# Kernel tuning notes

Hardware: AMD Instinct MI355X
Metric: run time of the kernel (lower is better)

Reference implementation:

```python
import jax, jax.numpy as jnp
import numpy as np

N = 50000   # nodes
E = 800000  # edges (avg degree 16)
F_IN = 128
H = 128
L = 4
LN_EPS = 1e-5


def setup_inputs() -> dict:
    key = jax.random.key(0)
    ks = jax.random.split(key, 4)
    x = jax.random.normal(ks[0], (N, F_IN), dtype=jnp.float32)
    edge_index = jax.random.randint(ks[1], (2, E), 0, N)
    conv_w = jax.random.normal(ks[2], (L, F_IN, H), dtype=jnp.float32) * 0.05
    conv_b = jnp.zeros((L, H), dtype=jnp.float32)
    ln_g = jnp.ones((L, H), dtype=jnp.float32)
    ln_b = jnp.zeros((L, H), dtype=jnp.float32)
    head_w = jax.random.normal(ks[3], (H, 1), dtype=jnp.float32) * 0.05
    head_b = jnp.zeros((1,), dtype=jnp.float32)
    return {"x": x, "edge_index": edge_index, "conv_w": conv_w, "conv_b": conv_b,
            "ln_g": ln_g, "ln_b": ln_b, "head_w": head_w, "head_b": head_b}


def _layer_norm(h, g, b):
    mu = jnp.mean(h, axis=-1, keepdims=True)
    var = jnp.mean(jnp.square(h - mu), axis=-1, keepdims=True)
    return (h - mu) * jax.lax.rsqrt(var + LN_EPS) * g + b


def _gcn_conv(h, W, b, src, dst, inv_sqrt_deg, inv_deg):
    # PyG GCNConv: self-loops + symmetric normalization D^-1/2 (A+I) D^-1/2, then bias.
    hw = h @ W  # (N, H)
    norm = inv_sqrt_deg[src] * inv_sqrt_deg[dst]  # (E,)
    msg = hw[src] * norm[:, None]  # gather + edgewise scale
    agg = jax.ops.segment_sum(msg, dst, num_segments=N)  # scatter-add
    agg = agg + hw * inv_deg[:, None]  # self-loop term (norm = 1/deg)
    return agg + b


def reference(x, edge_index, conv_w, conv_b, ln_g, ln_b, head_w, head_b):
    src, dst = edge_index[0], edge_index[1]
    # degree on target nodes, including self-loop
    deg = jax.ops.segment_sum(jnp.ones((E,), x.dtype), dst, num_segments=N) + 1.0
    inv_sqrt_deg = jax.lax.rsqrt(deg)
    inv_deg = 1.0 / deg
    h = x
    for i in range(L):
        h = _gcn_conv(h, conv_w[i], conv_b[i], src, dst, inv_sqrt_deg, inv_deg)
        h = _layer_norm(h, ln_g[i], ln_b[i])
        if i != L - 1:
            h = jax.nn.gelu(h, approximate=False)
            # dropout is identity in eval mode
    scores = (h @ head_w + head_b).squeeze(-1)  # (N,)
    return scores, h
```

## Files before the change

kernel.cpp:

```cpp
#include <hip/hip_runtime.h>
#include <math.h>

#define N_NODES 50000
#define N_EDGES 800000
#define HDIM 128
#define NLAYERS 4
#define LN_EPS 1e-5f
#define EHALF (N_EDGES / 2)
#define SEG 64
#define FILLB ((EHALF + 255) / 256)
#define GEMMB ((N_NODES + 63) / 64)
#define LFB ((N_NODES + 31) / 32)

typedef __attribute__((ext_vector_type(8))) short short8;
typedef __attribute__((ext_vector_type(4))) float floatx4;

__device__ __forceinline__ ushort f2bf(float x) {
    unsigned b = __float_as_uint(x);
    unsigned r = b + 0x7fffu + ((b >> 16) & 1u);
    return (ushort)(r >> 16);
}
__device__ __forceinline__ float2 bf2f2(unsigned u) {
    return make_float2(__uint_as_float(u << 16), __uint_as_float(u & 0xffff0000u));
}

__global__ __launch_bounds__(256) void prep_kernel(const float* __restrict__ W,
                                                   ushort* __restrict__ bfrag,
                                                   int* __restrict__ cnt) {
    int idx = blockIdx.x * 256 + threadIdx.x;
    if (idx < N_NODES) cnt[idx] = 0;
    if (idx < NLAYERS * 4 * 8 * 64) {
        int lane = idx & 63;
        int t = (idx >> 6) & 7;
        int s = (idx >> 9) & 3;
        int l = idx >> 11;
        int n = t * 16 + (lane & 15);
        int kb = s * 32 + (lane >> 4) * 8;
        const float* Wl = W + (size_t)l * HDIM * HDIM;
        union { uint4 q; ushort u[8]; } o;
#pragma unroll
        for (int j = 0; j < 8; ++j) o.u[j] = f2bf(Wl[(size_t)(kb + j) * HDIM + n]);
        *(uint4*)&bfrag[(size_t)idx * 8] = o.q;
    }
}

__device__ __forceinline__ void fill_body(int bid, int tid, const int* __restrict__ src,
                                          const int* __restrict__ dst, int* __restrict__ cnt,
                                          ushort* __restrict__ csr16) {
    int t = bid * 256 + tid;
    if (t >= EHALF) return;
    int s0 = src[t],         d0 = dst[t];
    int s1 = src[t + EHALF], d1 = dst[t + EHALF];
    int p0 = atomicAdd(&cnt[d0], 1);
    int p1 = atomicAdd(&cnt[d1], 1);
    if (p0 < SEG) csr16[d0 * SEG + p0] = (ushort)s0;
    if (p1 < SEG) csr16[d1 * SEG + p1] = (ushort)s1;
}

template <bool A_FP32>
__device__ __forceinline__ void gemm_body(int bid, int tid, const void* __restrict__ Av,
                                          const ushort* __restrict__ bfrag,
                                          ushort* __restrict__ out) {
    int wave = tid >> 6, lane = tid & 63;
    int quad = lane >> 4, mrow = lane & 15;
    int rowBase = bid * 64 + wave * 16;
    int arow = rowBase + mrow;
    bool aok = arow < N_NODES;

    floatx4 acc[8];
#pragma unroll
    for (int t = 0; t < 8; ++t) acc[t] = (floatx4)0.f;

#pragma unroll
    for (int s = 0; s < 4; ++s) {
        union { short8 v; ushort u[8]; } af;
        if (A_FP32) {
            const float* A = (const float*)Av;
            if (aok) {
                const float* p = &A[(size_t)arow * HDIM + s * 32 + quad * 8];
#pragma unroll
                for (int j = 0; j < 8; ++j) af.u[j] = f2bf(p[j]);
            } else {
#pragma unroll
                for (int j = 0; j < 8; ++j) af.u[j] = 0;
            }
        } else {
            const ushort* A = (const ushort*)Av;
            if (aok) {
                af.v = *(const short8*)&A[(size_t)arow * HDIM + s * 32 + quad * 8];
            } else {
#pragma unroll
                for (int j = 0; j < 8; ++j) af.u[j] = 0;
            }
        }
#pragma unroll
        for (int t = 0; t < 8; ++t) {
            short8 bf = *(const short8*)&bfrag[(size_t)(((s * 8 + t) * 64) + lane) * 8];
            acc[t] = __builtin_amdgcn_mfma_f32_16x16x32_bf16(af.v, bf, acc[t], 0, 0, 0);
        }
    }
#pragma unroll
    for (int t = 0; t < 8; ++t) {
#pragma unroll
        for (int r = 0; r < 4; ++r) {
            int row = rowBase + quad * 4 + r;
            if (row < N_NODES) out[(size_t)row * HDIM + t * 16 + mrow] = f2bf(acc[t][r]);
        }
    }
}

__global__ __launch_bounds__(256) void fused0_kernel(
    const int* __restrict__ src, const int* __restrict__ dst, int* __restrict__ cnt,
    ushort* __restrict__ csr16, const float* __restrict__ x,
    const ushort* __restrict__ bfrag0, ushort* __restrict__ hw) {
    if (blockIdx.x < FILLB)
        fill_body(blockIdx.x, threadIdx.x, src, dst, cnt, csr16);
    else
        gemm_body<true>(blockIdx.x - FILLB, threadIdx.x, x, bfrag0, hw);
}

__global__ __launch_bounds__(256) void agg_ln_kernel(
    const uint2* __restrict__ hw2, const int* __restrict__ degcnt,
    const ushort* __restrict__ csr16, const float* __restrict__ conv_b,
    const float* __restrict__ ln_g, const float* __restrict__ ln_b,
    uint2* __restrict__ hout_bf, float* __restrict__ hout_f32,
    const float* __restrict__ head_w, const float* __restrict__ head_b,
    float* __restrict__ scores, int final_layer) {
    int wave = threadIdx.x >> 6;
    int lane = threadIdx.x & 63;
    int g = lane >> 5;
    int li = lane & 31;
    int n = blockIdx.x * 4 + wave;
    if (n >= N_NODES) return;
    int c = li * 4;

    int rawc = degcnt[n];
    float dsum = (float)rawc + 1.0f;
    float isd_n = rsqrtf(dsum);
    float ind_n = isd_n * isd_n;
    int rs = n * SEG;
    int deg = min(rawc, SEG);

    float e0 = 0.f, e1 = 0.f, e2 = 0.f, e3 = 0.f;
    int sj = 0;
    float wj = 0.f;
    if (lane < deg) sj = (int)csr16[rs + lane];
    {
        float w = rsqrtf((float)degcnt[sj] + 1.0f);
        wj = (lane < deg) ? w : 0.f;
    }
    for (int j = 0; j < deg; j += 8) {
#pragma unroll
        for (int t = 0; t < 4; ++t) {
            int idx = j + 2 * t + g;
            int s = __shfl(sj, idx);
            float w = __shfl(wj, idx);
            uint2 u = hw2[(size_t)s * 32 + li];
            float2 q0 = bf2f2(u.x), q1 = bf2f2(u.y);
            e0 = fmaf(q0.x, w, e0); e1 = fmaf(q0.y, w, e1);
            e2 = fmaf(q1.x, w, e2); e3 = fmaf(q1.y, w, e3);
        }
    }
    e0 += __shfl_xor(e0, 32); e1 += __shfl_xor(e1, 32);
    e2 += __shfl_xor(e2, 32); e3 += __shfl_xor(e3, 32);

    uint2 hv = hw2[(size_t)n * 32 + li];
    float2 h0 = bf2f2(hv.x), h1 = bf2f2(hv.y);
    float4 cb = *(const float4*)&conv_b[c];
    float a0 = fmaf(e0, isd_n, fmaf(h0.x, ind_n, cb.x));
    float a1 = fmaf(e1, isd_n, fmaf(h0.y, ind_n, cb.y));
    float a2 = fmaf(e2, isd_n, fmaf(h1.x, ind_n, cb.z));
    float a3 = fmaf(e3, isd_n, fmaf(h1.y, ind_n, cb.w));

    float sum = a0 + a1 + a2 + a3;
#pragma unroll
    for (int o = 1; o < 32; o <<= 1) sum += __shfl_xor(sum, o);
    float mu = sum * (1.0f / HDIM);
    float d0 = a0 - mu, d1 = a1 - mu, d2 = a2 - mu, d3 = a3 - mu;
    float vs = d0 * d0 + d1 * d1 + d2 * d2 + d3 * d3;
#pragma unroll
    for (int o = 1; o < 32; o <<= 1) vs += __shfl_xor(vs, o);
    float rstd = rsqrtf(vs * (1.0f / HDIM) + LN_EPS);
    float4 gv = *(const float4*)&ln_g[c];
    float4 bv = *(const float4*)&ln_b[c];
    float y0 = fmaf(d0 * rstd, gv.x, bv.x);
    float y1 = fmaf(d1 * rstd, gv.y, bv.y);
    float y2 = fmaf(d2 * rstd, gv.z, bv.z);
    float y3 = fmaf(d3 * rstd, gv.w, bv.w);

    if (!final_layer) {
#define GELU(v) ((v) = 0.5f * (v) * (1.0f + erff((v) * 0.70710678118654752f)))
        GELU(y0); GELU(y1); GELU(y2); GELU(y3);
#undef GELU
        if (g == 0) {
            uint2 ov;
            ov.x = (unsigned)f2bf(y0) | ((unsigned)f2bf(y1) << 16);
            ov.y = (unsigned)f2bf(y2) | ((unsigned)f2bf(y3) << 16);
            hout_bf[(size_t)n * 32 + li] = ov;
        }
    } else {
        if (g == 0)
            *(float4*)&hout_f32[(size_t)n * HDIM + c] = make_float4(y0, y1, y2, y3);
        float4 hwv = *(const float4*)&head_w[c];
        float p = y0 * hwv.x + y1 * hwv.y + y2 * hwv.z + y3 * hwv.w;
#pragma unroll
        for (int o = 1; o < 32; o <<= 1) p += __shfl_xor(p, o);
        if (lane == 0) scores[n] = p + head_b[0];
    }
}

__global__ __launch_bounds__(512) void layer_fused_kernel(
    const uint2* __restrict__ h2, const int* __restrict__ degcnt,
    const ushort* __restrict__ csr16, const ushort* __restrict__ bfrag,
    const float* __restrict__ conv_b, const float* __restrict__ ln_g,
    const float* __restrict__ ln_b, uint2* __restrict__ hout_bf,
    float* __restrict__ hout_f32, const float* __restrict__ head_w,
    const float* __restrict__ head_b, float* __restrict__ scores,
    int final_layer) {
    __shared__ float aggsf[32][132];
    int wave = threadIdx.x >> 6, lane = threadIdx.x & 63;
    int g = lane >> 5, li = lane & 31;

    int nodeBase = blockIdx.x * 32 + wave * 4;
    int cnt_c = 0, sj_c = 0;
    float wj_c = 0.f;
    if (nodeBase < N_NODES) {
        cnt_c = degcnt[nodeBase];
        int degp = min(cnt_c, SEG);
        int sraw = (int)csr16[nodeBase * SEG + lane];
        sj_c = (lane < degp) ? sraw : 0;
        float w = rsqrtf((float)degcnt[sj_c] + 1.0f);
        wj_c = (lane < degp) ? w : 0.f;
    }
    for (int it = 0; it < 4; ++it) {
        int n = nodeBase + it;
        int deg = min(cnt_c, SEG), sj = sj_c;
        float dsum = (float)cnt_c + 1.0f;
        float wj = wj_c;
        int cnt_nx = 0, sraw_nx = 0;
        if (it < 3 && (n + 1) < N_NODES) {
            cnt_nx = degcnt[n + 1];
            sraw_nx = (int)csr16[(n + 1) * SEG + lane];
        }
        float a0 = 0.f, a1 = 0.f, a2 = 0.f, a3 = 0.f;
        if (n < N_NODES) {
            float isd_n = rsqrtf(dsum);
            float ind_n = isd_n * isd_n;
            uint2 hv = h2[(size_t)n * 32 + li];
            float e0 = 0.f, e1 = 0.f, e2 = 0.f, e3 = 0.f;
            uint2 u[4];
#pragma unroll
            for (int t = 0; t < 4; ++t) {
                int s = __shfl(sj, 2 * t + g);
                u[t] = h2[(size_t)s * 32 + li];
            }
            for (int j = 0; j < deg; j += 8) {
                uint2 un[4];
                int jn = j + 8;
                bool more = jn < deg;
                if (more) {
#pragma unroll
                    for (int t = 0; t < 4; ++t) {
                        int s = __shfl(sj, jn + 2 * t + g);
                        un[t] = h2[(size_t)s * 32 + li];
                    }
                }
#pragma unroll
                for (int t = 0; t < 4; ++t) {
                    float w = __shfl(wj, j + 2 * t + g);
                    float2 q0 = bf2f2(u[t].x), q1 = bf2f2(u[t].y);
                    e0 = fmaf(q0.x, w, e0); e1 = fmaf(q0.y, w, e1);
                    e2 = fmaf(q1.x, w, e2); e3 = fmaf(q1.y, w, e3);
                }
                if (more) { u[0] = un[0]; u[1] = un[1]; u[2] = un[2]; u[3] = un[3]; }
            }
            e0 += __shfl_xor(e0, 32); e1 += __shfl_xor(e1, 32);
            e2 += __shfl_xor(e2, 32); e3 += __shfl_xor(e3, 32);
            float2 h0 = bf2f2(hv.x), h1v = bf2f2(hv.y);
            a0 = fmaf(e0, isd_n, h0.x * ind_n);
            a1 = fmaf(e1, isd_n, h0.y * ind_n);
            a2 = fmaf(e2, isd_n, h1v.x * ind_n);
            a3 = fmaf(e3, isd_n, h1v.y * ind_n);
        }
        if (g == 0)
            *(float4*)&aggsf[wave * 4 + it][li * 4] = make_float4(a0, a1, a2, a3);
        int degp = min(cnt_nx, SEG);
        cnt_c = cnt_nx;
        sj_c = (lane < degp) ? sraw_nx : 0;
        float w = rsqrtf((float)degcnt[sj_c] + 1.0f);
        wj_c = (lane < degp) ? w : 0.f;
    }
    __syncthreads();

    int quad = lane >> 4, mrow = lane & 15;
    int rtile = (wave >> 2) * 16;
    int cq2 = (wave & 3) * 2;
    floatx4 acc[2];
    acc[0] = (floatx4)0.f;
    acc[1] = (floatx4)0.f;
#pragma unroll
    for (int s = 0; s < 4; ++s) {
        const float* rowp = &aggsf[rtile + mrow][s * 32 + quad * 8];
        float4 pa = *(const float4*)rowp;
        float4 pb = *(const float4*)(rowp + 4);
        float p[8] = {pa.x, pa.y, pa.z, pa.w, pb.x, pb.y, pb.z, pb.w};
        union { short8 v; ushort u[8]; } hi, lo;
#pragma unroll
        for (int j = 0; j < 8; ++j) {
            ushort h = f2bf(p[j]);
            hi.u[j] = h;
            float hf = __uint_as_float((unsigned)h << 16);
            lo.u[j] = f2bf(p[j] - hf);
        }
#pragma unroll
        for (int t4 = 0; t4 < 2; ++t4) {
            int t = cq2 + t4;
            short8 bf = *(const short8*)&bfrag[(size_t)(((s * 8 + t) * 64) + lane) * 8];
            acc[t4] = __builtin_amdgcn_mfma_f32_16x16x32_bf16(lo.v, bf, acc[t4], 0, 0, 0);
            acc[t4] = __builtin_amdgcn_mfma_f32_16x16x32_bf16(hi.v, bf, acc[t4], 0, 0, 0);
        }
    }
    __syncthreads();

    {
        float cb[2];
#pragma unroll
        for (int t4 = 0; t4 < 2; ++t4) cb[t4] = conv_b[(cq2 + t4) * 16 + mrow];
#pragma unroll
        for (int t4 = 0; t4 < 2; ++t4)
#pragma unroll
            for (int r = 0; r < 4; ++r)
                aggsf[rtile + quad * 4 + r][(cq2 + t4) * 16 + mrow] = acc[t4][r] + cb[t4];
    }
    __syncthreads();

    int c = li * 4;
    float4 gv = *(const float4*)&ln_g[c];
    float4 bv = *(const float4*)&ln_b[c];
    float4 hwv = *(const float4*)&head_w[c];
    for (int it = 0; it < 4; ++it) {
        int row = wave * 4 + it;
        int n = blockIdx.x * 32 + row;
        if (n >= N_NODES) continue;
        float4 v = *(const float4*)&aggsf[row][c];
        float a0 = v.x, a1 = v.y, a2 = v.z, a3 = v.w;

        float sum = a0 + a1 + a2 + a3;
#pragma unroll
        for (int o = 1; o < 32; o <<= 1) sum += __shfl_xor(sum, o);
        float mu = sum * (1.0f / HDIM);
        float d0 = a0 - mu, d1 = a1 - mu, d2 = a2 - mu, d3 = a3 - mu;
        float vs = d0 * d0 + d1 * d1 + d2 * d2 + d3 * d3;
#pragma unroll
        for (int o = 1; o < 32; o <<= 1) vs += __shfl_xor(vs, o);
        float rstd = rsqrtf(vs * (1.0f / HDIM) + LN_EPS);
        float y0 = fmaf(d0 * rstd, gv.x, bv.x);
        float y1 = fmaf(d1 * rstd, gv.y, bv.y);
        float y2 = fmaf(d2 * rstd, gv.z, bv.z);
        float y3 = fmaf(d3 * rstd, gv.w, bv.w);

        if (!final_layer) {
#define GELU(v) ((v) = 0.5f * (v) * (1.0f + erff((v) * 0.70710678118654752f)))
            GELU(y0); GELU(y1); GELU(y2); GELU(y3);
#undef GELU
            if (g == 0) {
                uint2 ov;
                ov.x = (unsigned)f2bf(y0) | ((unsigned)f2bf(y1) << 16);
                ov.y = (unsigned)f2bf(y2) | ((unsigned)f2bf(y3) << 16);
                hout_bf[(size_t)n * 32 + li] = ov;
            }
        } else {
            if (g == 0)
                *(float4*)&hout_f32[(size_t)n * HDIM + c] = make_float4(y0, y1, y2, y3);
            float p = y0 * hwv.x + y1 * hwv.y + y2 * hwv.z + y3 * hwv.w;
#pragma unroll
            for (int o = 1; o < 32; o <<= 1) p += __shfl_xor(p, o);
            if (lane == 0) scores[n] = p + head_b[0];
        }
    }
}


extern "C" void kernel_launch(void* const* d_in, const int* in_sizes, int n_in,
                              void* d_out, int out_size, void* d_ws, size_t ws_size,
                              hipStream_t stream) {
    const float* x      = (const float*)d_in[0];
    const int*   eidx   = (const int*)d_in[1];
    const float* conv_w = (const float*)d_in[2];
    const float* conv_b = (const float*)d_in[3];
    const float* ln_g   = (const float*)d_in[4];
    const float* ln_b   = (const float*)d_in[5];
    const float* head_w = (const float*)d_in[6];
    const float* head_b = (const float*)d_in[7];
    float* out = (float*)d_out;

    const int* src = eidx;
    const int* dst = eidx + N_EDGES;

    char* ws = (char*)d_ws;
    size_t o = 0;
    auto alloc = [&](size_t elems) {
        void* p = ws + o * 4;
        o += (elems + 15) & ~(size_t)15;
        return p;
    };
    int*      cnt      = (int*)alloc(N_NODES);
    ushort*   csr16    = (ushort*)alloc((size_t)N_NODES * SEG / 2);
    ushort*   bfrag    = (ushort*)alloc(NLAYERS * 4 * 8 * 64 * 8 / 2);
    unsigned* hw       = (unsigned*)alloc((size_t)N_NODES * 64);
    unsigned* hbuf     = (unsigned*)alloc((size_t)N_NODES * 64);

    prep_kernel<<<(N_NODES + 255) / 256, 256, 0, stream>>>(conv_w, bfrag, cnt);
    fused0_kernel<<<FILLB + GEMMB, 256, 0, stream>>>(src, dst, cnt, csr16, x, bfrag,
                                                     (ushort*)hw);

    agg_ln_kernel<<<(N_NODES + 3) / 4, 256, 0, stream>>>(
        (const uint2*)hw, cnt, csr16,
        conv_b, ln_g, ln_b,
        (uint2*)hbuf, out + N_NODES, head_w, head_b, out, 0);

    const unsigned* hin = hbuf;
    unsigned* hnext = hw;
    for (int l = 1; l < NLAYERS; ++l) {
        const ushort* bl = bfrag + (size_t)l * 4 * 8 * 64 * 8;
        int fin = (l == NLAYERS - 1) ? 1 : 0;
        layer_fused_kernel<<<LFB, 512, 0, stream>>>(
            (const uint2*)hin, cnt, csr16, bl,
            conv_b + (size_t)l * HDIM, ln_g + (size_t)l * HDIM, ln_b + (size_t)l * HDIM,
            (uint2*)hnext, out + N_NODES, head_w, head_b, out, fin);
        const unsigned* tmp = hin;
        hin = hnext;
        hnext = (unsigned*)tmp;
    }
}
```

Baseline: 340.2 us.

## Fuse all GCN layers into one persistent cooperative kernel with grid sync

Replaces the four per-layer kernel launches with a single cooperative persistent kernel. Blocks pull 32-node tiles through an atomic work cursor and separate layers with grid.sync(). The intent is to remove launch gaps and tail effects between layers and to balance irregular degree work dynamically. In exchange the grid is capped by occupancy, grid-wide barriers are added, and if the cooperative launch fails the code falls back to the old per-layer launches.

New measurement: 622.3 us. 82.9% more time.

```diff
diff --git a/kernel.cpp b/kernel.cpp
--- a/kernel.cpp
+++ b/kernel.cpp
@@ -1,5 +1,8 @@
 #include <hip/hip_runtime.h>
+#include <hip/hip_cooperative_groups.h>
 #include <math.h>
+
+namespace cg = cooperative_groups;
 
 #define N_NODES 50000
 #define N_EDGES 800000
@@ -26,9 +29,11 @@
 
 __global__ __launch_bounds__(256) void prep_kernel(const float* __restrict__ W,
                                                    ushort* __restrict__ bfrag,
-                                                   int* __restrict__ cnt) {
+                                                   int* __restrict__ cnt,
+                                                   int* __restrict__ cursor) {
     int idx = blockIdx.x * 256 + threadIdx.x;
     if (idx < N_NODES) cnt[idx] = 0;
+    if (idx < NLAYERS) cursor[idx] = 0;
     if (idx < NLAYERS * 4 * 8 * 64) {
         int lane = idx & 63;
         int t = (idx >> 6) & 7;
@@ -117,6 +122,231 @@
         fill_body(blockIdx.x, threadIdx.x, src, dst, cnt, csr16);
     else
         gemm_body<true>(blockIdx.x - FILLB, threadIdx.x, x, bfrag0, hw);
+}
+
+__global__ __launch_bounds__(512) void layers_kernel(
+    unsigned* __restrict__ hw, unsigned* __restrict__ hbuf,
+    const int* __restrict__ degcnt, const ushort* __restrict__ csr16,
+    const ushort* __restrict__ bfrag, const float* __restrict__ conv_b,
+    const float* __restrict__ ln_g, const float* __restrict__ ln_b,
+    const float* __restrict__ head_w, const float* __restrict__ head_b,
+    float* __restrict__ out, int* __restrict__ cursor) {
+    cg::grid_group grid = cg::this_grid();
+    __shared__ float aggsf[32][132];
+    __shared__ int tile_s;
+    int wave = threadIdx.x >> 6, lane = threadIdx.x & 63;
+    int g = lane >> 5, li = lane & 31;
+    int quad = lane >> 4, mrow = lane & 15;
+    float* scores = out;
+    float* hout_f32 = out + N_NODES;
+
+    for (int l = 0; l < NLAYERS; ++l) {
+        const uint2* h2 = (const uint2*)((l & 1) ? hbuf : hw);
+        uint2* hnext = (uint2*)((l & 1) ? hw : hbuf);
+        const ushort* bfr = bfrag + (size_t)l * 4 * 8 * 64 * 8;
+        const float* cbL = conv_b + (size_t)l * HDIM;
+        const float* gL = ln_g + (size_t)l * HDIM;
+        const float* bL = ln_b + (size_t)l * HDIM;
+        int fin = (l == NLAYERS - 1);
+
+        for (;;) {
+            if (threadIdx.x == 0) tile_s = atomicAdd(&cursor[l], 1);
+            __syncthreads();
+            int tile = tile_s;
+            __syncthreads();
+            if (tile >= LFB) break;
+
+            int nodeBase = tile * 32 + wave * 4;
+            int cnt_c = 0, sj_c = 0;
+            float wj_c = 0.f;
+            if (nodeBase < N_NODES) {
+                cnt_c = degcnt[nodeBase];
+                int degp = min(cnt_c, SEG);
+                int sraw = (int)csr16[nodeBase * SEG + lane];
+                sj_c = (lane < degp) ? sraw : 0;
+                float w = rsqrtf((float)degcnt[sj_c] + 1.0f);
+                wj_c = (lane < degp) ? w : 0.f;
+            }
+            for (int it = 0; it < 4; ++it) {
+                int n = nodeBase + it;
+                int deg = min(cnt_c, SEG), sj = sj_c;
+                float dsum = (float)cnt_c + 1.0f;
+                float wj = wj_c;
+                int cnt_nx = 0, sraw_nx = 0;
+                if (it < 3 && (n + 1) < N_NODES) {
+                    cnt_nx = degcnt[n + 1];
+                    sraw_nx = (int)csr16[(n + 1) * SEG + lane];
+                }
+                float a0 = 0.f, a1 = 0.f, a2 = 0.f, a3 = 0.f;
+                if (n < N_NODES) {
+                    float isd_n = rsqrtf(dsum);
+                    float ind_n = isd_n * isd_n;
+                    uint2 hv = h2[(size_t)n * 32 + li];
+                    float e0 = 0.f, e1 = 0.f, e2 = 0.f, e3 = 0.f;
+                    uint2 u[4];
+#pragma unroll
+                    for (int t = 0; t < 4; ++t) {
+                        int s = __shfl(sj, 2 * t + g);
+                        u[t] = h2[(size_t)s * 32 + li];
+                    }
+                    for (int j = 0; j < deg; j += 8) {
+                        uint2 un[4];
+                        int jn = j + 8;
+                        bool more = jn < deg;
+                        if (more) {
+#pragma unroll
+                            for (int t = 0; t < 4; ++t) {
+                                int s = __shfl(sj, jn + 2 * t + g);
+                                un[t] = h2[(size_t)s * 32 + li];
+                            }
+                        }
+#pragma unroll
+                        for (int t = 0; t < 4; ++t) {
+                            float w = __shfl(wj, j + 2 * t + g);
+                            float2 q0 = bf2f2(u[t].x), q1 = bf2f2(u[t].y);
+                            e0 = fmaf(q0.x, w, e0); e1 = fmaf(q0.y, w, e1);
+                            e2 = fmaf(q1.x, w, e2); e3 = fmaf(q1.y, w, e3);
+                        }
+                        if (more) { u[0] = un[0]; u[1] = un[1]; u[2] = un[2]; u[3] = un[3]; }
+                    }
+                    e0 += __shfl_xor(e0, 32); e1 += __shfl_xor(e1, 32);
+                    e2 += __shfl_xor(e2, 32); e3 += __shfl_xor(e3, 32);
+                    float2 h0 = bf2f2(hv.x), h1v = bf2f2(hv.y);
+                    a0 = fmaf(e0, isd_n, h0.x * ind_n);
+                    a1 = fmaf(e1, isd_n, h0.y * ind_n);
+                    a2 = fmaf(e2, isd_n, h1v.x * ind_n);
+                    a3 = fmaf(e3, isd_n, h1v.y * ind_n);
+                }
+                if (l == 0) {
+                    if (n < N_NODES) {
+                        int c = li * 4;
+                        float4 cb4 = *(const float4*)&cbL[c];
+                        a0 += cb4.x; a1 += cb4.y; a2 += cb4.z; a3 += cb4.w;
+                        float sum = a0 + a1 + a2 + a3;
+#pragma unroll
+                        for (int o2 = 1; o2 < 32; o2 <<= 1) sum += __shfl_xor(sum, o2);
+                        float mu = sum * (1.0f / HDIM);
+                        float d0 = a0 - mu, d1 = a1 - mu, d2 = a2 - mu, d3 = a3 - mu;
+                        float vs = d0 * d0 + d1 * d1 + d2 * d2 + d3 * d3;
+#pragma unroll
+                        for (int o2 = 1; o2 < 32; o2 <<= 1) vs += __shfl_xor(vs, o2);
+                        float rstd = rsqrtf(vs * (1.0f / HDIM) + LN_EPS);
+                        float4 gv = *(const float4*)&gL[c];
+                        float4 bv = *(const float4*)&bL[c];
+                        float y0 = fmaf(d0 * rstd, gv.x, bv.x);
+                        float y1 = fmaf(d1 * rstd, gv.y, bv.y);
+                        float y2 = fmaf(d2 * rstd, gv.z, bv.z);
+                        float y3 = fmaf(d3 * rstd, gv.w, bv.w);
+#define GELU(v) ((v) = 0.5f * (v) * (1.0f + erff((v) * 0.70710678118654752f)))
+                        GELU(y0); GELU(y1); GELU(y2); GELU(y3);
+#undef GELU
+                        if (g == 0) {
+                            uint2 ov;
+                            ov.x = (unsigned)f2bf(y0) | ((unsigned)f2bf(y1) << 16);
+                            ov.y = (unsigned)f2bf(y2) | ((unsigned)f2bf(y3) << 16);
+                            hnext[(size_t)n * 32 + li] = ov;
+                        }
+                    }
+                } else {
+                    if (g == 0)
+                        *(float4*)&aggsf[wave * 4 + it][li * 4] = make_float4(a0, a1, a2, a3);
+                }
+                int degp = min(cnt_nx, SEG);
+                cnt_c = cnt_nx;
+                sj_c = (lane < degp) ? sraw_nx : 0;
+                float w = rsqrtf((float)degcnt[sj_c] + 1.0f);
+                wj_c = (lane < degp) ? w : 0.f;
+            }
+            if (l == 0) continue;
+
+            __syncthreads();
+
+            int rtile = (wave >> 2) * 16;
+            int cq2 = (wave & 3) * 2;
+            floatx4 acc[2];
+            acc[0] = (floatx4)0.f;
+            acc[1] = (floatx4)0.f;
+#pragma unroll
+            for (int s = 0; s < 4; ++s) {
+                const float* rowp = &aggsf[rtile + mrow][s * 32 + quad * 8];
+                float4 pa = *(const float4*)rowp;
+                float4 pb = *(const float4*)(rowp + 4);
+                float p[8] = {pa.x, pa.y, pa.z, pa.w, pb.x, pb.y, pb.z, pb.w};
+                union { short8 v; ushort u[8]; } hi, lo;
+#pragma unroll
+                for (int j = 0; j < 8; ++j) {
+                    ushort h = f2bf(p[j]);
+                    hi.u[j] = h;
+                    float hf = __uint_as_float((unsigned)h << 16);
+                    lo.u[j] = f2bf(p[j] - hf);
+                }
+#pragma unroll
+                for (int t4 = 0; t4 < 2; ++t4) {
+                    int t = cq2 + t4;
+                    short8 bf = *(const short8*)&bfr[(size_t)(((s * 8 + t) * 64) + lane) * 8];
+                    acc[t4] = __builtin_amdgcn_mfma_f32_16x16x32_bf16(lo.v, bf, acc[t4], 0, 0, 0);
+                    acc[t4] = __builtin_amdgcn_mfma_f32_16x16x32_bf16(hi.v, bf, acc[t4], 0, 0, 0);
+                }
+            }
+            __syncthreads();
+
+            {
+                float cb[2];
+#pragma unroll
+                for (int t4 = 0; t4 < 2; ++t4) cb[t4] = cbL[(cq2 + t4) * 16 + mrow];
+#pragma unroll
+                for (int t4 = 0; t4 < 2; ++t4)
+#pragma unroll
+                    for (int r = 0; r < 4; ++r)
+                        aggsf[rtile + quad * 4 + r][(cq2 + t4) * 16 + mrow] = acc[t4][r] + cb[t4];
+            }
+            __syncthreads();
+
+            int c = li * 4;
+            float4 gv = *(const float4*)&gL[c];
+            float4 bv = *(const float4*)&bL[c];
+            float4 hwv = *(const float4*)&head_w[c];
+            for (int it = 0; it < 4; ++it) {
+                int row = wave * 4 + it;
+                int n = tile * 32 + row;
+                if (n >= N_NODES) continue;
+                float4 v = *(const float4*)&aggsf[row][c];
+                float a0 = v.x, a1 = v.y, a2 = v.z, a3 = v.w;
+                float sum = a0 + a1 + a2 + a3;
+#pragma unroll
+                for (int o2 = 1; o2 < 32; o2 <<= 1) sum += __shfl_xor(sum, o2);
+                float mu = sum * (1.0f / HDIM);
+                float d0 = a0 - mu, d1 = a1 - mu, d2 = a2 - mu, d3 = a3 - mu;
+                float vs = d0 * d0 + d1 * d1 + d2 * d2 + d3 * d3;
+#pragma unroll
+                for (int o2 = 1; o2 < 32; o2 <<= 1) vs += __shfl_xor(vs, o2);
+                float rstd = rsqrtf(vs * (1.0f / HDIM) + LN_EPS);
+                float y0 = fmaf(d0 * rstd, gv.x, bv.x);
+                float y1 = fmaf(d1 * rstd, gv.y, bv.y);
+                float y2 = fmaf(d2 * rstd, gv.z, bv.z);
+                float y3 = fmaf(d3 * rstd, gv.w, bv.w);
+                if (!fin) {
+#define GELU(v) ((v) = 0.5f * (v) * (1.0f + erff((v) * 0.70710678118654752f)))
+                    GELU(y0); GELU(y1); GELU(y2); GELU(y3);
+#undef GELU
+                    if (g == 0) {
+                        uint2 ov;
+                        ov.x = (unsigned)f2bf(y0) | ((unsigned)f2bf(y1) << 16);
+                        ov.y = (unsigned)f2bf(y2) | ((unsigned)f2bf(y3) << 16);
+                        hnext[(size_t)n * 32 + li] = ov;
+                    }
+                } else {
+                    if (g == 0)
+                        *(float4*)&hout_f32[(size_t)n * HDIM + c] = make_float4(y0, y1, y2, y3);
+                    float p = y0 * hwv.x + y1 * hwv.y + y2 * hwv.z + y3 * hwv.w;
+#pragma unroll
+                    for (int o2 = 1; o2 < 32; o2 <<= 1) p += __shfl_xor(p, o2);
+                    if (lane == 0) scores[n] = p + head_b[0];
+                }
+            }
+        }
+        grid.sync();
+    }
 }
 
 __global__ __launch_bounds__(256) void agg_ln_kernel(
@@ -405,31 +635,61 @@
         return p;
     };
     int*      cnt      = (int*)alloc(N_NODES);
+    int*      cursor   = (int*)alloc(16);
     ushort*   csr16    = (ushort*)alloc((size_t)N_NODES * SEG / 2);
     ushort*   bfrag    = (ushort*)alloc(NLAYERS * 4 * 8 * 64 * 8 / 2);
     unsigned* hw       = (unsigned*)alloc((size_t)N_NODES * 64);
     unsigned* hbuf     = (unsigned*)alloc((size_t)N_NODES * 64);
 
-    prep_kernel<<<(N_NODES + 255) / 256, 256, 0, stream>>>(conv_w, bfrag, cnt);
+    prep_kernel<<<(N_NODES + 255) / 256, 256, 0, stream>>>(conv_w, bfrag, cnt, cursor);
     fused0_kernel<<<FILLB + GEMMB, 256, 0, stream>>>(src, dst, cnt, csr16, x, bfrag,
                                                      (ushort*)hw);
 
-    agg_ln_kernel<<<(N_NODES + 3) / 4, 256, 0, stream>>>(
-        (const uint2*)hw, cnt, csr16,
-        conv_b, ln_g, ln_b,
-        (uint2*)hbuf, out + N_NODES, head_w, head_b, out, 0);
-
-    const unsigned* hin = hbuf;
-    unsigned* hnext = hw;
-    for (int l = 1; l < NLAYERS; ++l) {
-        const ushort* bl = bfrag + (size_t)l * 4 * 8 * 64 * 8;
-        int fin = (l == NLAYERS - 1) ? 1 : 0;
-        layer_fused_kernel<<<LFB, 512, 0, stream>>>(
-            (const uint2*)hin, cnt, csr16, bl,
-            conv_b + (size_t)l * HDIM, ln_g + (size_t)l * HDIM, ln_b + (size_t)l * HDIM,
-            (uint2*)hnext, out + N_NODES, head_w, head_b, out, fin);
-        const unsigned* tmp = hin;
-        hin = hnext;
-        hnext = (unsigned*)tmp;
-    }
-}
+    static int coopGrid = 0;
+    if (coopGrid == 0) {
+        int mpc = 0;
+        hipError_t qe = hipOccupancyMaxActiveBlocksPerMultiprocessor(
+            &mpc, (const void*)layers_kernel, 512, 0);
+        if (qe != hipSuccess || mpc < 1) mpc = 1;
+        long gmax = (long)mpc * 256;
+        if (gmax > LFB) gmax = LFB;
+        if (gmax < 1) gmax = 1;
+        coopGrid = (int)gmax;
+    }
+    unsigned* a0_ = hw;
+    unsigned* a1_ = hbuf;
+    const int* a2_ = cnt;
+    const ushort* a3_ = csr16;
+    const ushort* a4_ = bfrag;
+    const float* a5_ = conv_b;
+    const float* a6_ = ln_g;
+    const float* a7_ = ln_b;
+    const float* a8_ = head_w;
+    const float* a9_ = head_b;
+    float* a10_ = out;
+    int* a11_ = cursor;
+    void* kargs[] = {&a0_, &a1_, &a2_, &a3_, &a4_, &a5_,
+                     &a6_, &a7_, &a8_, &a9_, &a10_, &a11_};
+    hipError_t le = hipLaunchCooperativeKernel((const void*)layers_kernel,
+                                               dim3(coopGrid), dim3(512),
+                                               kargs, 0, stream);
+    if (le != hipSuccess) {
+        agg_ln_kernel<<<(N_NODES + 3) / 4, 256, 0, stream>>>(
+            (const uint2*)hw, cnt, csr16, conv_b, ln_g, ln_b,
+            (uint2*)hbuf, out + N_NODES, head_w, head_b, out, 0);
+        const unsigned* hin = hbuf;
+        unsigned* hnext = hw;
+        for (int l = 1; l < NLAYERS; ++l) {
+            const ushort* bl = bfrag + (size_t)l * 4 * 8 * 64 * 8;
+            int fin = (l == NLAYERS - 1) ? 1 : 0;
+            layer_fused_kernel<<<LFB, 512, 0, stream>>>(
+                (const uint2*)hin, cnt, csr16, bl,
+                conv_b + (size_t)l * HDIM, ln_g + (size_t)l * HDIM,
+                ln_b + (size_t)l * HDIM,
+                (uint2*)hnext, out + N_NODES, head_w, head_b, out, fin);
+            const unsigned* tmp = hin;
+            hin = hnext;
+            hnext = (unsigned*)tmp;
+        }
+    }
+}
```
